# Performance work log

Measured on AMD Instinct MI355X. Metric: run time of the kernel, lower is better.

The kernel has to match this reference:

```python
import jax, jax.numpy as jnp
import numpy as np


def conv1x1(x, w, b):
    # x: [B,C,H,W], w: [O,C], b: [O] -> [B,O,H,W]
    return jnp.einsum('bchw,oc->bohw', x, w) + b[None, :, None, None]


def maxpool2x2(x):
    B, C, H, W = x.shape
    return x.reshape(B, C, H // 2, 2, W // 2, 2).max(axis=(3, 5))


def setup_inputs() -> dict:
    key = jax.random.key(0)
    ks = jax.random.split(key, 10)
    C = 256
    x = jax.random.normal(ks[0], (16, C, 64, 64), dtype=jnp.float32)
    s = lambda fan_in: 1.0 / np.sqrt(fan_in)
    w_theta = jax.random.normal(ks[1], (C // 8, C), dtype=jnp.float32) * s(C)
    b_theta = jax.random.normal(ks[2], (C // 8,), dtype=jnp.float32) * 0.01
    w_phi = jax.random.normal(ks[3], (C // 8, C), dtype=jnp.float32) * s(C)
    b_phi = jax.random.normal(ks[4], (C // 8,), dtype=jnp.float32) * 0.01
    w_g = jax.random.normal(ks[5], (C // 2, C), dtype=jnp.float32) * s(C)
    b_g = jax.random.normal(ks[6], (C // 2,), dtype=jnp.float32) * 0.01
    w_attn = jax.random.normal(ks[7], (C, C // 2), dtype=jnp.float32) * s(C // 2)
    b_attn = jax.random.normal(ks[8], (C,), dtype=jnp.float32) * 0.01
    sigma = jnp.full((1,), 0.5, dtype=jnp.float32)
    return {"x": x, "w_theta": w_theta, "b_theta": b_theta,
            "w_phi": w_phi, "b_phi": b_phi, "w_g": w_g, "b_g": b_g,
            "w_attn": w_attn, "b_attn": b_attn, "sigma": sigma}


def reference(x, w_theta, b_theta, w_phi, b_phi, w_g, b_g, w_attn, b_attn, sigma):
    B, C, W, H = x.shape
    N = W * H
    N4 = N // 4
    # Q: [B, N, C/8]
    theta = conv1x1(x, w_theta, b_theta).reshape(B, C // 8, N).transpose(0, 2, 1)
    # K: [B, C/8, N/4] (2x2 maxpool downsample)
    phi = maxpool2x2(conv1x1(x, w_phi, b_phi)).reshape(B, C // 8, N4)
    # attention: [B, N, N/4]
    attn = jax.nn.softmax(jnp.einsum('bnc,bcm->bnm', theta, phi), axis=-1)
    # V: [B, N/4, C/2]
    g = maxpool2x2(conv1x1(x, w_g, b_g)).reshape(B, C // 2, N4).transpose(0, 2, 1)
    attn_g = jnp.einsum('bnm,bmc->bnc', attn, g).transpose(0, 2, 1).reshape(B, C // 2, W, H)
    attn_g = conv1x1(attn_g, w_attn, b_attn)
    return x + sigma[0] * attn_g
```

## Files before the change

### kernel.cpp

```cpp
#include <hip/hip_runtime.h>
#include <math.h>

#define BATCH 16
#define CIN   256
#define NPIX  4096
#define NP4   1024
#define DQK   32
#define DV    128
#define QW    32
#define QT    128

typedef __attribute__((ext_vector_type(8)))  short short8v;
typedef __attribute__((ext_vector_type(16))) float f32x16;

#define ZERO16 {0.f,0.f,0.f,0.f,0.f,0.f,0.f,0.f,0.f,0.f,0.f,0.f,0.f,0.f,0.f,0.f}
#define LOG2E 1.44269504088896340736f
#define MFIX 64.0f

__device__ __forceinline__ unsigned short f2bf(float f) {
    unsigned u = __float_as_uint(f);
    u += 0x7FFFu + ((u >> 16) & 1u);
    return (unsigned short)(u >> 16);
}

__device__ __forceinline__ unsigned cvtpk(float a, float b) {
    unsigned r;
    asm("v_cvt_pk_bf16_f32 %0, %1, %2" : "=v"(r) : "v"(a), "v"(b));
    return r;
}

__device__ __forceinline__ short8v ldg8(const unsigned short* p) {
    return *(const short8v*)p;
}

#define PLSWAP(a, b) asm("v_permlane32_swap_b32 %0, %1" : "+v"(a), "+v"(b))

__global__ void wcvt_k(const float* __restrict__ wt, const float* __restrict__ wp,
                       const float* __restrict__ wg, const float* __restrict__ wa,
                       unsigned short* __restrict__ wqkv, unsigned short* __restrict__ wab)
{
    int i = blockIdx.x * 256 + threadIdx.x;
    if (i < 192 * 256) {
        int row = i >> 8, c = i & 255;
        float v = row < 32 ? wt[row * 256 + c]
                : row < 64 ? wp[(row - 32) * 256 + c]
                           : wg[(row - 64) * 256 + c];
        wqkv[i] = f2bf(v);
    } else {
        int j = i - 192 * 256;
        if (j < 256 * DV) wab[j] = f2bf(wa[j]);
    }
}

__global__ __launch_bounds__(256, 2) void conv_qkv_k(
    const float* __restrict__ x, const unsigned short* __restrict__ wqkv,
    const float* __restrict__ b_theta, const float* __restrict__ b_phi,
    const float* __restrict__ b_g, unsigned short* __restrict__ Qg,
    unsigned short* __restrict__ Kg, unsigned short* __restrict__ Vg)
{
    __shared__ __align__(16) union {
        unsigned short xs[2][2][128][8];
        float pool[2][160][32];
    } u;

    const int b    = blockIdx.y;
    const int tile = blockIdx.x;
    const int pixb = tile * 128;
    const int t    = threadIdx.x;
    const int wv   = t >> 6, l = t & 63, h = l >> 5, q31 = l & 31;
    const int sp   = t & 127, skb = t >> 7;

    const float* xb = x + (size_t)b * CIN * NPIX + pixb + sp;

    f32x16 acc[6];
#pragma unroll
    for (int i = 0; i < 6; ++i) acc[i] = ZERO16;

    float xa[8], xbr[8];
#pragma unroll
    for (int j = 0; j < 8; ++j) xa[j] = xb[(size_t)(skb * 8 + j) * NPIX];
    {
        unsigned pk[4];
#pragma unroll
        for (int jj = 0; jj < 4; ++jj) pk[jj] = cvtpk(xa[2*jj], xa[2*jj+1]);
        *(uint4*)&u.xs[0][skb][sp][0] = *(uint4*)pk;
    }
#pragma unroll
    for (int j = 0; j < 8; ++j) xbr[j] = xb[(size_t)(16 + skb * 8 + j) * NPIX];
    __syncthreads();

    for (int ks = 0; ks < 16; ks += 2) {
        if (ks < 14) {
            const float* xn = xb + (size_t)((ks + 2) * 16 + skb * 8) * NPIX;
#pragma unroll
            for (int j = 0; j < 8; ++j) xa[j] = xn[(size_t)j * NPIX];
        }
        {
            short8v bf = *(const short8v*)&u.xs[0][h][wv * 32 + q31][0];
#pragma unroll
            for (int rb = 0; rb < 6; ++rb) {
                short8v af = *(const short8v*)&wqkv[(size_t)(rb * 32 + q31) * 256 + ks * 16 + h * 8];
                acc[rb] = __builtin_amdgcn_mfma_f32_32x32x16_bf16(af, bf, acc[rb], 0, 0, 0);
            }
        }
        {
            unsigned pk[4];
#pragma unroll
            for (int jj = 0; jj < 4; ++jj) pk[jj] = cvtpk(xbr[2*jj], xbr[2*jj+1]);
            *(uint4*)&u.xs[1][skb][sp][0] = *(uint4*)pk;
        }
        __syncthreads();

        if (ks < 14) {
            const float* xn = xb + (size_t)((ks + 3) * 16 + skb * 8) * NPIX;
#pragma unroll
            for (int j = 0; j < 8; ++j) xbr[j] = xn[(size_t)j * NPIX];
        }
        {
            short8v bf = *(const short8v*)&u.xs[1][h][wv * 32 + q31][0];
#pragma unroll
            for (int rb = 0; rb < 6; ++rb) {
                short8v af = *(const short8v*)&wqkv[(size_t)(rb * 32 + q31) * 256 + (ks + 1) * 16 + h * 8];
                acc[rb] = __builtin_amdgcn_mfma_f32_32x32x16_bf16(af, bf, acc[rb], 0, 0, 0);
            }
        }
        if (ks < 14) {
            unsigned pk[4];
#pragma unroll
            for (int jj = 0; jj < 4; ++jj) pk[jj] = cvtpk(xa[2*jj], xa[2*jj+1]);
            *(uint4*)&u.xs[0][skb][sp][0] = *(uint4*)pk;
        }
        __syncthreads();
    }

    {
        int pix = pixb + wv * 32 + q31;
        unsigned short* qout = &Qg[((size_t)b * NPIX + pix) * DQK];
#pragma unroll
        for (int m = 0; m < 4; ++m) {
            unsigned pk2[2];
            float v0 = (acc[0][m*4+0] + b_theta[4*h + 8*m + 0]) * LOG2E;
            float v1 = (acc[0][m*4+1] + b_theta[4*h + 8*m + 1]) * LOG2E;
            float v2 = (acc[0][m*4+2] + b_theta[4*h + 8*m + 2]) * LOG2E;
            float v3 = (acc[0][m*4+3] + b_theta[4*h + 8*m + 3]) * LOG2E;
            pk2[0] = cvtpk(v0, v1);
            pk2[1] = cvtpk(v2, v3);
            *(uint2*)&qout[8*m + 4*h] = *(uint2*)pk2;
        }
    }

#pragma unroll
    for (int rb = 1; rb < 6; ++rb) {
#pragma unroll
        for (int r = 0; r < 16; ++r) {
            float v  = acc[rb][r];
            float o  = __shfl_xor(v, 1);
            float mx = fmaxf(v, o);
            if ((q31 & 1) == 0) {
                int row = (r & 3) + 8 * (r >> 2) + 4 * h;
                u.pool[wv >> 1][(rb - 1) * 32 + row][(wv & 1) * 16 + (q31 >> 1)] = mx;
            }
        }
    }
    __syncthreads();

    {
        int wx = t & 31;
        int pp = tile * 32 + wx;
#pragma unroll
        for (int i = 0; i < 20; ++i) {
            int ch = (t >> 5) * 20 + i;
            float v = fmaxf(u.pool[0][ch][wx], u.pool[1][ch][wx]);
            if (ch < 32) {
                v += b_phi[ch];
                Kg[(((size_t)b * 4 + (ch >> 3)) * NP4 + pp) * 8 + (ch & 7)] = f2bf(v);
            } else {
                int c = ch - 32;
                v += b_g[c];
                Vg[((size_t)b * 128 + (pp >> 3)) * (DV * 8) + (size_t)c * 8 + (pp & 7)] = f2bf(v);
            }
        }
    }
}

__global__ __launch_bounds__(256, 2) void flash_k(
    const unsigned short* __restrict__ Qg, const unsigned short* __restrict__ Kg,
    const unsigned short* __restrict__ Vg, const unsigned short* __restrict__ wab,
    const float* __restrict__ b_attn, const float* __restrict__ sigma,
    const float* __restrict__ x, float* __restrict__ out)
{
    __shared__ __align__(16) unsigned short os[4][16 * 33 * 8];
    __shared__ __align__(16) float ls[32][132];

    const int b    = blockIdx.y;
    const int t    = threadIdx.x;
    const int wv   = t >> 6;
    const int l    = t & 63;
    const int h    = l >> 5;
    const int q31  = l & 31;
    const int pxblk = blockIdx.x * QT;
    const int p0   = pxblk + wv * QW;

    const unsigned short* Kp = Kg + (size_t)b * 4 * NP4 * 8 + ((size_t)h * NP4 + q31) * 8;
    const unsigned short* Vp = Vg + (size_t)b * 128 * DV * 8 + h * 1024 + q31 * 8;

    short8v qf0 = ldg8(&Qg[((size_t)b * NPIX + p0 + q31) * DQK + h * 8]);
    short8v qf1 = ldg8(&Qg[((size_t)b * NPIX + p0 + q31) * DQK + 16 + h * 8]);

    f32x16 o0 = ZERO16, o1 = ZERO16, o2 = ZERO16, o3 = ZERO16;
    float lsum = 0.f;

    short8v kfA[4], kfB[4], vg[16];
#pragma unroll
    for (int i = 0; i < 4; ++i)
        kfA[i] = ldg8(Kp + (i >> 1) * (2 * NP4 * 8) + (i & 1) * 256);
#pragma unroll
    for (int g = 0; g < 4; ++g)
#pragma unroll
        for (int cc = 0; cc < 4; ++cc)
            vg[g * 4 + cc] = ldg8(Vp + g * 2048 + cc * 256);

    auto tile = [&](int kt, short8v (&kfc)[4], short8v (&kfn)[4], bool pref) {
        f32x16 s0 = ZERO16, s1 = ZERO16;
        s0 = __builtin_amdgcn_mfma_f32_32x32x16_bf16(kfc[0], qf0, s0, 0, 0, 0);
        s1 = __builtin_amdgcn_mfma_f32_32x32x16_bf16(kfc[1], qf0, s1, 0, 0, 0);
        s0 = __builtin_amdgcn_mfma_f32_32x32x16_bf16(kfc[2], qf1, s0, 0, 0, 0);
        s1 = __builtin_amdgcn_mfma_f32_32x32x16_bf16(kfc[3], qf1, s1, 0, 0, 0);

        if (pref) {
            const unsigned short* kp1 = Kp + (size_t)(kt + 1) * 512;
#pragma unroll
            for (int i = 0; i < 4; ++i)
                kfn[i] = ldg8(kp1 + (i >> 1) * (2 * NP4 * 8) + (i & 1) * 256);
        }

        float ts[16];
#pragma unroll
        for (int r = 0; r < 16; ++r) {
            s0[r] = exp2f(s0[r] - MFIX);
            s1[r] = exp2f(s1[r] - MFIX);
            ts[r] = s0[r] + s1[r];
        }
#pragma unroll
        for (int d = 8; d >= 1; d >>= 1)
#pragma unroll
            for (int r = 0; r < d; ++r) ts[r] += ts[r + d];
        lsum += ts[0] + __shfl_xor(ts[0], 32);

        unsigned ca[8], cb[8];
#pragma unroll
        for (int j = 0; j < 8; ++j) {
            ca[j] = cvtpk(s0[2*j], s0[2*j+1]);
            cb[j] = cvtpk(s1[2*j], s1[2*j+1]);
        }
        PLSWAP(ca[0], ca[2]); PLSWAP(ca[1], ca[3]);
        PLSWAP(ca[4], ca[6]); PLSWAP(ca[5], ca[7]);
        PLSWAP(cb[0], cb[2]); PLSWAP(cb[1], cb[3]);
        PLSWAP(cb[4], cb[6]); PLSWAP(cb[5], cb[7]);
        union { unsigned uu[4]; short8v v; } pa[4];
#pragma unroll
        for (int j = 0; j < 4; ++j) {
            pa[0].uu[j] = ca[j];     pa[1].uu[j] = ca[4 + j];
            pa[2].uu[j] = cb[j];     pa[3].uu[j] = cb[4 + j];
        }

        const unsigned short* vp1 = Vp + (size_t)(kt + 1) * 8192;
#pragma unroll
        for (int g = 0; g < 4; ++g) {
            o0 = __builtin_amdgcn_mfma_f32_32x32x16_bf16(pa[g].v, vg[g*4+0], o0, 0, 0, 0);
            o1 = __builtin_amdgcn_mfma_f32_32x32x16_bf16(pa[g].v, vg[g*4+1], o1, 0, 0, 0);
            o2 = __builtin_amdgcn_mfma_f32_32x32x16_bf16(pa[g].v, vg[g*4+2], o2, 0, 0, 0);
            o3 = __builtin_amdgcn_mfma_f32_32x32x16_bf16(pa[g].v, vg[g*4+3], o3, 0, 0, 0);
            if (pref) {
#pragma unroll
                for (int cc = 0; cc < 4; ++cc)
                    vg[g*4+cc] = ldg8(vp1 + g * 2048 + cc * 256);
            }
        }
    };

    for (int kt = 0; kt < 16; kt += 2) {
        tile(kt,     kfA, kfB, true);
        tile(kt + 1, kfB, kfA, kt + 1 < 15);
    }

    float rinv = 1.0f / lsum;
    unsigned short* osw = os[wv];
#pragma unroll
    for (int r = 0; r < 16; ++r) {
        int q = (r & 3) + 8 * (r >> 2) + 4 * h;
        float rn = __shfl(rinv, q);
        int e8 = l & 7;
        osw[(((q31 >> 3)     ) * 33 + q) * 8 + e8] = f2bf(o0[r] * rn);
        osw[(((q31 >> 3) +  4) * 33 + q) * 8 + e8] = f2bf(o1[r] * rn);
        osw[(((q31 >> 3) +  8) * 33 + q) * 8 + e8] = f2bf(o2[r] * rn);
        osw[(((q31 >> 3) + 12) * 33 + q) * 8 + e8] = f2bf(o3[r] * rn);
    }

    const float sg = sigma[0];
    const int cl8  = t >> 5;
    const int px4  = (t & 31) * 4;
#pragma unroll 1
    for (int cht = 0; cht < 8; ++cht) {
        float4 xv[4];
#pragma unroll
        for (int rep = 0; rep < 4; ++rep) {
            int ch = cht * 32 + rep * 8 + cl8;
            xv[rep] = *(const float4*)&x[((size_t)b * 256 + ch) * NPIX + pxblk + px4];
        }

        f32x16 e = ZERO16;
#pragma unroll
        for (int ks16 = 0; ks16 < 8; ++ks16) {
            short8v wf = ldg8(&wab[(size_t)(cht * 32 + q31) * DV + ks16 * 16 + h * 8]);
            short8v of = *(const short8v*)&osw[((ks16 * 2 + h) * 33 + q31) * 8];
            e = __builtin_amdgcn_mfma_f32_32x32x16_bf16(wf, of, e, 0, 0, 0);
        }
#pragma unroll
        for (int r = 0; r < 16; ++r) {
            int crow = (r & 3) + 8 * (r >> 2) + 4 * h;
            ls[crow][wv * 32 + q31] = e[r];
        }
        __syncthreads();
#pragma unroll
        for (int rep = 0; rep < 4; ++rep) {
            int cl = rep * 8 + cl8;
            int ch = cht * 32 + cl;
            float4 v = *(const float4*)&ls[cl][px4];
            float bias = b_attn[ch];
            size_t idx = ((size_t)b * 256 + ch) * NPIX + pxblk + px4;
            float4 o;
            o.x = fmaf(sg, v.x + bias, xv[rep].x);
            o.y = fmaf(sg, v.y + bias, xv[rep].y);
            o.z = fmaf(sg, v.z + bias, xv[rep].z);
            o.w = fmaf(sg, v.w + bias, xv[rep].w);
            *(float4*)&out[idx] = o;
        }
        __syncthreads();
    }
}

extern "C" void kernel_launch(void* const* d_in, const int* in_sizes, int n_in,
                              void* d_out, int out_size, void* d_ws, size_t ws_size,
                              hipStream_t stream) {
    const float* x       = (const float*)d_in[0];
    const float* w_theta = (const float*)d_in[1];
    const float* b_theta = (const float*)d_in[2];
    const float* w_phi   = (const float*)d_in[3];
    const float* b_phi   = (const float*)d_in[4];
    const float* w_g     = (const float*)d_in[5];
    const float* b_g     = (const float*)d_in[6];
    const float* w_attn  = (const float*)d_in[7];
    const float* b_attn  = (const float*)d_in[8];
    const float* sigma   = (const float*)d_in[9];
    float* out = (float*)d_out;

    unsigned short* Qg   = (unsigned short*)d_ws;
    unsigned short* Kg   = Qg + (size_t)BATCH * NPIX * DQK;
    unsigned short* Vg   = Kg + (size_t)BATCH * 4 * NP4 * 8;
    unsigned short* wab  = Vg + (size_t)BATCH * 128 * DV * 8;
    unsigned short* wqkv = wab + (size_t)256 * DV;

    wcvt_k    <<<dim3((192 * 256 + 256 * DV + 255) / 256), 256, 0, stream>>>(
        w_theta, w_phi, w_g, w_attn, wqkv, wab);
    conv_qkv_k<<<dim3(NPIX / 128, BATCH), 256, 0, stream>>>(
        x, wqkv, b_theta, b_phi, b_g, Qg, Kg, Vg);
    flash_k   <<<dim3(NPIX / QT, BATCH), 256, 0, stream>>>(
        Qg, Kg, Vg, wab, b_attn, sigma, x, out);
}
```

Baseline: 104.4 us.

## Double-buffer epilogue staging and prefetch next residual tile of x

The output-projection epilogue now ping-pongs between two LDS staging buffers, which lets it drop the trailing barrier in each channel-tile iteration. It also software-pipelines the residual x loads, prefetching the next 32-channel tile while the current MFMA and store run. The loop is fully unrolled. This costs extra LDS (a second 32x132 float buffer) and more registers for the doubled x prefetch, which could lower occupancy under the 2-blocks-per-SM launch bound.

Measured after the change: 102.7 us. Within noise of the previous version (-1.6%).

```diff
diff --git a/kernel.cpp b/kernel.cpp
--- a/kernel.cpp
+++ b/kernel.cpp
@@ -190,7 +190,7 @@
     const float* __restrict__ x, float* __restrict__ out)
 {
     __shared__ __align__(16) unsigned short os[4][16 * 33 * 8];
-    __shared__ __align__(16) float ls[32][132];
+    __shared__ __align__(16) float ls[2][32][132];
 
     const int b    = blockIdx.y;
     const int t    = threadIdx.x;
@@ -297,46 +297,56 @@
         osw[(((q31 >> 3) + 12) * 33 + q) * 8 + e8] = f2bf(o3[r] * rn);
     }
 
-    const float sg = sigma[0];
-    const int cl8  = t >> 5;
-    const int px4  = (t & 31) * 4;
-#pragma unroll 1
+    const float sg  = sigma[0];
+    const int  cl8  = t >> 5;
+    const int  px4  = (t & 31) * 4;
+
+    float4 xv[2][4];
+#pragma unroll
+    for (int rep = 0; rep < 4; ++rep) {
+        int ch = rep * 8 + cl8;
+        xv[0][rep] = *(const float4*)&x[((size_t)b * 256 + ch) * NPIX + pxblk + px4];
+    }
+
+#pragma unroll
     for (int cht = 0; cht < 8; ++cht) {
-        float4 xv[4];
-#pragma unroll
-        for (int rep = 0; rep < 4; ++rep) {
-            int ch = cht * 32 + rep * 8 + cl8;
-            xv[rep] = *(const float4*)&x[((size_t)b * 256 + ch) * NPIX + pxblk + px4];
+        const int cur = cht & 1;
+        if (cht < 7) {
+#pragma unroll
+            for (int rep = 0; rep < 4; ++rep) {
+                int ch = (cht + 1) * 32 + rep * 8 + cl8;
+                xv[cur ^ 1][rep] =
+                    *(const float4*)&x[((size_t)b * 256 + ch) * NPIX + pxblk + px4];
+            }
         }
 
         f32x16 e = ZERO16;
 #pragma unroll
         for (int ks16 = 0; ks16 < 8; ++ks16) {
-            short8v wf = ldg8(&wab[(size_t)(cht * 32 + q31) * DV + ks16 * 16 + h * 8]);
-            short8v of = *(const short8v*)&osw[((ks16 * 2 + h) * 33 + q31) * 8];
-            e = __builtin_amdgcn_mfma_f32_32x32x16_bf16(wf, of, e, 0, 0, 0);
+            short8v wfv = ldg8(&wab[(size_t)(cht * 32 + q31) * DV + ks16 * 16 + h * 8]);
+            short8v of  = *(const short8v*)&osw[((ks16 * 2 + h) * 33 + q31) * 8];
+            e = __builtin_amdgcn_mfma_f32_32x32x16_bf16(wfv, of, e, 0, 0, 0);
         }
 #pragma unroll
         for (int r = 0; r < 16; ++r) {
             int crow = (r & 3) + 8 * (r >> 2) + 4 * h;
-            ls[crow][wv * 32 + q31] = e[r];
+            ls[cur][crow][wv * 32 + q31] = e[r];
         }
         __syncthreads();
 #pragma unroll
         for (int rep = 0; rep < 4; ++rep) {
             int cl = rep * 8 + cl8;
             int ch = cht * 32 + cl;
-            float4 v = *(const float4*)&ls[cl][px4];
+            float4 v = *(const float4*)&ls[cur][cl][px4];
             float bias = b_attn[ch];
             size_t idx = ((size_t)b * 256 + ch) * NPIX + pxblk + px4;
             float4 o;
-            o.x = fmaf(sg, v.x + bias, xv[rep].x);
-            o.y = fmaf(sg, v.y + bias, xv[rep].y);
-            o.z = fmaf(sg, v.z + bias, xv[rep].z);
-            o.w = fmaf(sg, v.w + bias, xv[rep].w);
+            o.x = fmaf(sg, v.x + bias, xv[cur][rep].x);
+            o.y = fmaf(sg, v.y + bias, xv[cur][rep].y);
+            o.z = fmaf(sg, v.z + bias, xv[cur][rep].z);
+            o.w = fmaf(sg, v.w + bias, xv[cur][rep].w);
             *(float4*)&out[idx] = o;
         }
-        __syncthreads();
     }
 }
 
```
